# Performance work log

Measured on AMD Instinct MI355X. Metric: run time of the kernel, lower is better.

Reference implementation:

```python
import jax, jax.numpy as jnp
import numpy as np

B, N, H, HID, P = 4, 1024, 16, 64, 2


def setup_inputs() -> dict:
    key = jax.random.key(0)
    ks = jax.random.split(key, 8)
    positions = jax.random.normal(ks[0], (B, N, P), dtype=jnp.float32)
    key_padding_mask = jax.random.bernoulli(ks[1], 0.1, (B, N))
    # MLP params (Linear stores weight as (out,in) in torch; we keep (in,out) and matmul)
    s1 = 1.0 / np.sqrt(P)
    s2 = 1.0 / np.sqrt(HID)
    W1 = jax.random.uniform(ks[2], (P, HID), jnp.float32, -s1, s1)
    b1 = jax.random.uniform(ks[3], (HID,), jnp.float32, -s1, s1)
    W2 = jax.random.uniform(ks[4], (HID, HID), jnp.float32, -s2, s2)
    b2 = jax.random.uniform(ks[5], (HID,), jnp.float32, -s2, s2)
    W3 = jax.random.uniform(ks[6], (HID, H), jnp.float32, -s2, s2)
    b3 = jax.random.uniform(ks[7], (H,), jnp.float32, -s2, s2)
    return {"positions": positions, "key_padding_mask": key_padding_mask,
            "W1": W1, "b1": b1, "W2": W2, "b2": b2, "W3": W3, "b3": b3}


def reference(positions, key_padding_mask, W1, b1, W2, b2, W3, b3):
    # rel_pos[b, i, j] = pos[b, j] - pos[b, i]  -> (B, N, N, 2)
    rel = positions[:, None, :, :] - positions[:, :, None, :]
    h = jax.nn.relu(rel @ W1 + b1)          # (B, N, N, HID)
    h = jax.nn.relu(h @ W2 + b2)            # (B, N, N, HID)
    bias = h @ W3 + b3                      # (B, N, N, H)
    bias = jnp.transpose(bias, (0, 3, 1, 2))  # (B, H, N, N)
    # zero out rows/cols touching padded tokens
    combined = key_padding_mask[:, None, None, :] | key_padding_mask[:, None, :, None]
    bias = jnp.where(combined, 0.0, bias)
    return bias
```

## Files before the change

### kernel.cpp

```cpp
#include <hip/hip_runtime.h>
#include <hip/hip_bf16.h>
#include <hip/hip_fp16.h>

#define B_   4
#define N_   1024
#define H_   16
#define HID_ 64
#define TI   16
#define TJ   128
#define USJ  36

typedef float    f32x4  __attribute__((ext_vector_type(4)));
typedef __fp16   fp16x2 __attribute__((ext_vector_type(2)));
typedef _Float16 f16x8  __attribute__((ext_vector_type(8)));
typedef unsigned int u32;

union F16x8U { u32 u[4]; f16x8 v; };

static __device__ __forceinline__ u32 pk(float a, float b) {
    union { fp16x2 f; u32 u; } r;
    r.f = __builtin_amdgcn_cvt_pkrtz(a, b);
    return r.u;
}
static __device__ __forceinline__ u32 pkadd_relu(u32 a, u32 b) {
    union { u32 u; fp16x2 f; } x, y, r;
    x.u = a; y.u = b;
    fp16x2 z = { (__fp16)0.f, (__fp16)0.f };
    fp16x2 s = x.f + y.f;
    r.f = __builtin_elementwise_max(s, z);
    return r.u;
}
static __device__ __forceinline__ u32 pkcvt_relu(float a, float b) {
    union { fp16x2 f; u32 u; } r;
    fp16x2 z = { (__fp16)0.f, (__fp16)0.f };
    fp16x2 s = __builtin_amdgcn_cvt_pkrtz(a, b);
    r.f = __builtin_elementwise_max(s, z);
    return r.u;
}

__global__ __launch_bounds__(256) void RelativePositionalBias_kernel(
    const float* __restrict__ pos,
    const int*   __restrict__ mask,
    const float* __restrict__ W1,
    const float* __restrict__ b1,
    const float* __restrict__ W2,
    const float* __restrict__ b2,
    const float* __restrict__ W3,
    const float* __restrict__ b3,
    float* __restrict__ out)
{
    __shared__ __align__(16) u32 ujL[TJ][USJ];
    __shared__ __align__(16) u32 uinL[TI][USJ];

    const int b  = blockIdx.z;
    const int i0 = blockIdx.y * TI;
    const int j0 = blockIdx.x * TJ;
    const int tid = threadIdx.x;
    const int w = tid >> 6;
    const int l = tid & 63;
    const int g = l >> 4;
    const int c = l & 15;

    for (int it = tid; it < (TJ + TI) * 8; it += 256) {
        int r  = it >> 3;
        int qq = (it & 7) * 4;
        int k0 = qq * 2;
        int tok = (r < TJ) ? (j0 + r) : (i0 + (r - TJ));
        float2 p  = *(const float2*)&pos[(b * N_ + tok) * 2];
        float4 a0 = *(const float4*)&W1[k0];
        float4 a1 = *(const float4*)&W1[k0 + 4];
        float4 c0 = *(const float4*)&W1[HID_ + k0];
        float4 c1 = *(const float4*)&W1[HID_ + k0 + 4];
        float u0 = p.x*a0.x + p.y*c0.x, u1 = p.x*a0.y + p.y*c0.y;
        float u2 = p.x*a0.z + p.y*c0.z, u3 = p.x*a0.w + p.y*c0.w;
        float u4 = p.x*a1.x + p.y*c1.x, u5 = p.x*a1.y + p.y*c1.y;
        float u6 = p.x*a1.z + p.y*c1.z, u7 = p.x*a1.w + p.y*c1.w;
        uint4 o;
        if (r < TJ) {
            o.x = pk(u0, u1); o.y = pk(u2, u3); o.z = pk(u4, u5); o.w = pk(u6, u7);
            *(uint4*)&ujL[r][qq] = o;
        } else {
            float4 ba = *(const float4*)&b1[k0];
            float4 bb = *(const float4*)&b1[k0 + 4];
            o.x = pk(ba.x - u0, ba.y - u1); o.y = pk(ba.z - u2, ba.w - u3);
            o.z = pk(bb.x - u4, bb.y - u5); o.w = pk(bb.z - u6, bb.w - u7);
            *(uint4*)&uinL[r - TJ][qq] = o;
        }
    }

    F16x8U W2f[2][4];
    #pragma unroll
    for (int s = 0; s < 2; ++s)
        #pragma unroll
        for (int n = 0; n < 4; ++n)
            #pragma unroll
            for (int e = 0; e < 8; ++e)
                W2f[s][n].v[e] = (_Float16)W2[(32*s + 8*g + e) * HID_ + 16*n + c];

    F16x8U W3g[2];
    #pragma unroll
    for (int s = 0; s < 2; ++s)
        #pragma unroll
        for (int e = 0; e < 8; ++e)
            W3g[s].v[e] = (_Float16)W3[(32*s + 16*(e>>2) + 4*g + (e&3)) * H_ + c];

    f32x4 b2v[4];
    #pragma unroll
    for (int n = 0; n < 4; ++n)
        b2v[n] = *(const f32x4*)&b2[16*n + 4*g];

    const float b3v = b3[c];
    const int* maskb = &mask[b * N_ + i0];
    const int4 mj0 = *(const int4*)&mask[b * N_ + j0 + 32*w + 4*g];
    const int4 mj1 = *(const int4*)&mask[b * N_ + j0 + 32*w + 16 + 4*g];
    float* const outBase = out + ((size_t)(b*H_ + c) << 20) + (size_t)(j0 + 32*w + 4*g)
                               + ((size_t)i0 << 10);

    __syncthreads();

    const uint4 pj00 = *(const uint4*)&ujL[32*w + c][4*g];
    const uint4 pj01 = *(const uint4*)&ujL[32*w + c][16 + 4*g];
    const uint4 pj10 = *(const uint4*)&ujL[32*w + 16 + c][4*g];
    const uint4 pj11 = *(const uint4*)&ujL[32*w + 16 + c][16 + 4*g];

    #pragma unroll 2
    for (int t = 0; t < TI; ++t) {
        const int mi = maskb[t];
        float* const outRow = outBase + ((size_t)t << 10);
        f32x4 o0 = { 0.f, 0.f, 0.f, 0.f };
        f32x4 o1 = { 0.f, 0.f, 0.f, 0.f };

        if (!mi) {
            const uint4 uiA = *(const uint4*)&uinL[t][4*g];
            const uint4 uiB = *(const uint4*)&uinL[t][16 + 4*g];

            #pragma unroll
            for (int u = 0; u < 2; ++u) {
                const uint4& pjA = u ? pj10 : pj00;
                const uint4& pjB = u ? pj11 : pj01;

                F16x8U A1[2];
                A1[0].u[0] = pkadd_relu(pjA.x, uiA.x);
                A1[0].u[1] = pkadd_relu(pjA.y, uiA.y);
                A1[0].u[2] = pkadd_relu(pjA.z, uiA.z);
                A1[0].u[3] = pkadd_relu(pjA.w, uiA.w);
                A1[1].u[0] = pkadd_relu(pjB.x, uiB.x);
                A1[1].u[1] = pkadd_relu(pjB.y, uiB.y);
                A1[1].u[2] = pkadd_relu(pjB.z, uiB.z);
                A1[1].u[3] = pkadd_relu(pjB.w, uiB.w);

                f32x4 acc[4];
                #pragma unroll
                for (int n = 0; n < 4; ++n) {
                    acc[n] = __builtin_amdgcn_mfma_f32_16x16x32_f16(W2f[0][n].v, A1[0].v, b2v[n], 0, 0, 0);
                    acc[n] = __builtin_amdgcn_mfma_f32_16x16x32_f16(W2f[1][n].v, A1[1].v, acc[n], 0, 0, 0);
                }

                F16x8U A3[2];
                #pragma unroll
                for (int s = 0; s < 2; ++s) {
                    A3[s].u[0] = pkcvt_relu(acc[2*s][0],     acc[2*s][1]);
                    A3[s].u[1] = pkcvt_relu(acc[2*s][2],     acc[2*s][3]);
                    A3[s].u[2] = pkcvt_relu(acc[2*s + 1][0], acc[2*s + 1][1]);
                    A3[s].u[3] = pkcvt_relu(acc[2*s + 1][2], acc[2*s + 1][3]);
                }

                f32x4 acc3 = { b3v, b3v, b3v, b3v };
                acc3 = __builtin_amdgcn_mfma_f32_16x16x32_f16(A3[0].v, W3g[0].v, acc3, 0, 0, 0);
                acc3 = __builtin_amdgcn_mfma_f32_16x16x32_f16(A3[1].v, W3g[1].v, acc3, 0, 0, 0);

                const int4& mj = u ? mj1 : mj0;
                f32x4& o = u ? o1 : o0;
                o[0] = mj.x ? 0.f : acc3[0];
                o[1] = mj.y ? 0.f : acc3[1];
                o[2] = mj.z ? 0.f : acc3[2];
                o[3] = mj.w ? 0.f : acc3[3];
            }
        }

        *(f32x4*)(outRow)      = o0;
        *(f32x4*)(outRow + 16) = o1;
    }
}

extern "C" void kernel_launch(void* const* d_in, const int* in_sizes, int n_in,
                              void* d_out, int out_size, void* d_ws, size_t ws_size,
                              hipStream_t stream) {
    const float* pos  = (const float*)d_in[0];
    const int*   mask = (const int*)d_in[1];
    const float* W1   = (const float*)d_in[2];
    const float* b1   = (const float*)d_in[3];
    const float* W2   = (const float*)d_in[4];
    const float* b2   = (const float*)d_in[5];
    const float* W3   = (const float*)d_in[6];
    const float* b3   = (const float*)d_in[7];
    float* out = (float*)d_out;

    dim3 grid(N_ / TJ, N_ / TI, B_);
    RelativePositionalBias_kernel<<<grid, dim3(256), 0, stream>>>(
        pos, mask, W1, b1, W2, b2, W3, b3, out);
}
```

Measured before the change: 62.58 us.

## Widen block to full j-row with swizzled LDS layout and bitmask masking

Each block now covers all 1024 j tokens for 16 i rows, using 512 threads. The full j-side layer-1 projections are staged in LDS with an XOR swizzle instead of padding, which cuts the number of blocks and the repeated per-block setup of W2/W3 register fragments. Row masks are packed into a bitmask and column masks become multiplicative factors, and rows where the i token is padded skip straight to zero stores. The trade-offs are larger LDS use (about 130KB), fewer blocks (256) and a request for 2 blocks per CU, which may limit occupancy and make the tail of the grid uneven.

```diff
diff --git a/kernel.cpp b/kernel.cpp
--- a/kernel.cpp
+++ b/kernel.cpp
@@ -7,8 +7,6 @@
 #define H_   16
 #define HID_ 64
 #define TI   16
-#define TJ   128
-#define USJ  36
 
 typedef float    f32x4  __attribute__((ext_vector_type(4)));
 typedef __fp16   fp16x2 __attribute__((ext_vector_type(2)));
@@ -38,7 +36,7 @@
     return r.u;
 }
 
-__global__ __launch_bounds__(256) void RelativePositionalBias_kernel(
+__global__ __launch_bounds__(512, 2) void RelativePositionalBias_kernel(
     const float* __restrict__ pos,
     const int*   __restrict__ mask,
     const float* __restrict__ W1,
@@ -49,23 +47,22 @@
     const float* __restrict__ b3,
     float* __restrict__ out)
 {
-    __shared__ __align__(16) u32 ujL[TJ][USJ];
-    __shared__ __align__(16) u32 uinL[TI][USJ];
-
-    const int b  = blockIdx.z;
-    const int i0 = blockIdx.y * TI;
-    const int j0 = blockIdx.x * TJ;
+    __shared__ __align__(16) u32 ujL[N_][32];
+    __shared__ __align__(16) u32 uinL[TI][32];
+
+    const int b   = blockIdx.y;
+    const int i0  = blockIdx.x * TI;
     const int tid = threadIdx.x;
     const int w = tid >> 6;
     const int l = tid & 63;
     const int g = l >> 4;
     const int c = l & 15;
 
-    for (int it = tid; it < (TJ + TI) * 8; it += 256) {
+    for (int it = tid; it < (N_ + TI) * 8; it += 512) {
         int r  = it >> 3;
-        int qq = (it & 7) * 4;
-        int k0 = qq * 2;
-        int tok = (r < TJ) ? (j0 + r) : (i0 + (r - TJ));
+        int qq = it & 7;
+        int k0 = qq * 8;
+        int tok = (r < N_) ? r : (i0 + (r - N_));
         float2 p  = *(const float2*)&pos[(b * N_ + tok) * 2];
         float4 a0 = *(const float4*)&W1[k0];
         float4 a1 = *(const float4*)&W1[k0 + 4];
@@ -75,16 +72,17 @@
         float u2 = p.x*a0.z + p.y*c0.z, u3 = p.x*a0.w + p.y*c0.w;
         float u4 = p.x*a1.x + p.y*c1.x, u5 = p.x*a1.y + p.y*c1.y;
         float u6 = p.x*a1.z + p.y*c1.z, u7 = p.x*a1.w + p.y*c1.w;
+        const int col = ((qq ^ (r & 7)) << 2);
         uint4 o;
-        if (r < TJ) {
+        if (r < N_) {
             o.x = pk(u0, u1); o.y = pk(u2, u3); o.z = pk(u4, u5); o.w = pk(u6, u7);
-            *(uint4*)&ujL[r][qq] = o;
+            *(uint4*)&ujL[r][col] = o;
         } else {
             float4 ba = *(const float4*)&b1[k0];
             float4 bb = *(const float4*)&b1[k0 + 4];
             o.x = pk(ba.x - u0, ba.y - u1); o.y = pk(ba.z - u2, ba.w - u3);
             o.z = pk(bb.x - u4, bb.y - u5); o.w = pk(bb.z - u6, bb.w - u7);
-            *(uint4*)&uinL[r - TJ][qq] = o;
+            *(uint4*)&uinL[r - N_][col] = o;
         }
     }
 
@@ -108,78 +106,89 @@
     #pragma unroll
     for (int n = 0; n < 4; ++n)
         b2v[n] = *(const f32x4*)&b2[16*n + 4*g];
-
     const float b3v = b3[c];
+
     const int* maskb = &mask[b * N_ + i0];
-    const int4 mj0 = *(const int4*)&mask[b * N_ + j0 + 32*w + 4*g];
-    const int4 mj1 = *(const int4*)&mask[b * N_ + j0 + 32*w + 16 + 4*g];
-    float* const outBase = out + ((size_t)(b*H_ + c) << 20) + (size_t)(j0 + 32*w + 4*g)
-                               + ((size_t)i0 << 10);
+    u32 mrow = 0;
+    #pragma unroll
+    for (int tt = 0; tt < 4; ++tt) {
+        int4 m = *(const int4*)&maskb[tt * 4];
+        mrow |= (m.x ? 1u : 0u) << (4*tt);
+        mrow |= (m.y ? 1u : 0u) << (4*tt + 1);
+        mrow |= (m.z ? 1u : 0u) << (4*tt + 2);
+        mrow |= (m.w ? 1u : 0u) << (4*tt + 3);
+    }
+
+    f32x4 mmul[8];
+    #pragma unroll
+    for (int jj = 0; jj < 8; ++jj) {
+        int4 mj = *(const int4*)&mask[b * N_ + 128*w + 16*jj + 4*g];
+        mmul[jj][0] = mj.x ? 0.f : 1.f;
+        mmul[jj][1] = mj.y ? 0.f : 1.f;
+        mmul[jj][2] = mj.z ? 0.f : 1.f;
+        mmul[jj][3] = mj.w ? 0.f : 1.f;
+    }
+
+    float* const planeBase = out + ((size_t)(b*H_ + c) << 20) + ((size_t)i0 << 10)
+                                 + (size_t)(128*w + 4*g);
 
     __syncthreads();
 
-    const uint4 pj00 = *(const uint4*)&ujL[32*w + c][4*g];
-    const uint4 pj01 = *(const uint4*)&ujL[32*w + c][16 + 4*g];
-    const uint4 pj10 = *(const uint4*)&ujL[32*w + 16 + c][4*g];
-    const uint4 pj11 = *(const uint4*)&ujL[32*w + 16 + c][16 + 4*g];
-
-    #pragma unroll 2
+    const f32x4 zero4 = { 0.f, 0.f, 0.f, 0.f };
+
     for (int t = 0; t < TI; ++t) {
-        const int mi = maskb[t];
-        float* const outRow = outBase + ((size_t)t << 10);
-        f32x4 o0 = { 0.f, 0.f, 0.f, 0.f };
-        f32x4 o1 = { 0.f, 0.f, 0.f, 0.f };
-
-        if (!mi) {
-            const uint4 uiA = *(const uint4*)&uinL[t][4*g];
-            const uint4 uiB = *(const uint4*)&uinL[t][16 + 4*g];
-
-            #pragma unroll
-            for (int u = 0; u < 2; ++u) {
-                const uint4& pjA = u ? pj10 : pj00;
-                const uint4& pjB = u ? pj11 : pj01;
-
-                F16x8U A1[2];
-                A1[0].u[0] = pkadd_relu(pjA.x, uiA.x);
-                A1[0].u[1] = pkadd_relu(pjA.y, uiA.y);
-                A1[0].u[2] = pkadd_relu(pjA.z, uiA.z);
-                A1[0].u[3] = pkadd_relu(pjA.w, uiA.w);
-                A1[1].u[0] = pkadd_relu(pjB.x, uiB.x);
-                A1[1].u[1] = pkadd_relu(pjB.y, uiB.y);
-                A1[1].u[2] = pkadd_relu(pjB.z, uiB.z);
-                A1[1].u[3] = pkadd_relu(pjB.w, uiB.w);
-
-                f32x4 acc[4];
-                #pragma unroll
-                for (int n = 0; n < 4; ++n) {
-                    acc[n] = __builtin_amdgcn_mfma_f32_16x16x32_f16(W2f[0][n].v, A1[0].v, b2v[n], 0, 0, 0);
-                    acc[n] = __builtin_amdgcn_mfma_f32_16x16x32_f16(W2f[1][n].v, A1[1].v, acc[n], 0, 0, 0);
-                }
-
-                F16x8U A3[2];
-                #pragma unroll
-                for (int s = 0; s < 2; ++s) {
-                    A3[s].u[0] = pkcvt_relu(acc[2*s][0],     acc[2*s][1]);
-                    A3[s].u[1] = pkcvt_relu(acc[2*s][2],     acc[2*s][3]);
-                    A3[s].u[2] = pkcvt_relu(acc[2*s + 1][0], acc[2*s + 1][1]);
-                    A3[s].u[3] = pkcvt_relu(acc[2*s + 1][2], acc[2*s + 1][3]);
-                }
-
-                f32x4 acc3 = { b3v, b3v, b3v, b3v };
-                acc3 = __builtin_amdgcn_mfma_f32_16x16x32_f16(A3[0].v, W3g[0].v, acc3, 0, 0, 0);
-                acc3 = __builtin_amdgcn_mfma_f32_16x16x32_f16(A3[1].v, W3g[1].v, acc3, 0, 0, 0);
-
-                const int4& mj = u ? mj1 : mj0;
-                f32x4& o = u ? o1 : o0;
-                o[0] = mj.x ? 0.f : acc3[0];
-                o[1] = mj.y ? 0.f : acc3[1];
-                o[2] = mj.z ? 0.f : acc3[2];
-                o[3] = mj.w ? 0.f : acc3[3];
+        float* const rowp = planeBase + ((size_t)t << 10);
+
+        if ((mrow >> t) & 1) {
+            #pragma unroll
+            for (int jj = 0; jj < 8; ++jj)
+                *(f32x4*)(rowp + 16*jj) = zero4;
+            continue;
+        }
+
+        const int tb = t & 7;
+        const uint4 uiA = *(const uint4*)&uinL[t][(g ^ tb) << 2];
+        const uint4 uiB = *(const uint4*)&uinL[t][((4 + g) ^ tb) << 2];
+
+        #pragma unroll
+        for (int jj = 0; jj < 8; ++jj) {
+            const int jrow = 128*w + 16*jj + c;
+            const int jb = c & 7;
+            const uint4 pjA = *(const uint4*)&ujL[jrow][(g ^ jb) << 2];
+            const uint4 pjB = *(const uint4*)&ujL[jrow][((4 + g) ^ jb) << 2];
+
+            F16x8U A1[2];
+            A1[0].u[0] = pkadd_relu(pjA.x, uiA.x);
+            A1[0].u[1] = pkadd_relu(pjA.y, uiA.y);
+            A1[0].u[2] = pkadd_relu(pjA.z, uiA.z);
+            A1[0].u[3] = pkadd_relu(pjA.w, uiA.w);
+            A1[1].u[0] = pkadd_relu(pjB.x, uiB.x);
+            A1[1].u[1] = pkadd_relu(pjB.y, uiB.y);
+            A1[1].u[2] = pkadd_relu(pjB.z, uiB.z);
+            A1[1].u[3] = pkadd_relu(pjB.w, uiB.w);
+
+            f32x4 acc[4];
+            #pragma unroll
+            for (int n = 0; n < 4; ++n) {
+                acc[n] = __builtin_amdgcn_mfma_f32_16x16x32_f16(W2f[0][n].v, A1[0].v, b2v[n], 0, 0, 0);
+                acc[n] = __builtin_amdgcn_mfma_f32_16x16x32_f16(W2f[1][n].v, A1[1].v, acc[n], 0, 0, 0);
             }
+
+            F16x8U A3[2];
+            #pragma unroll
+            for (int s = 0; s < 2; ++s) {
+                A3[s].u[0] = pkcvt_relu(acc[2*s][0],     acc[2*s][1]);
+                A3[s].u[1] = pkcvt_relu(acc[2*s][2],     acc[2*s][3]);
+                A3[s].u[2] = pkcvt_relu(acc[2*s + 1][0], acc[2*s + 1][1]);
+                A3[s].u[3] = pkcvt_relu(acc[2*s + 1][2], acc[2*s + 1][3]);
+            }
+
+            f32x4 acc3 = { b3v, b3v, b3v, b3v };
+            acc3 = __builtin_amdgcn_mfma_f32_16x16x32_f16(A3[0].v, W3g[0].v, acc3, 0, 0, 0);
+            acc3 = __builtin_amdgcn_mfma_f32_16x16x32_f16(A3[1].v, W3g[1].v, acc3, 0, 0, 0);
+
+            *(f32x4*)(rowp + 16*jj) = acc3 * mmul[jj];
         }
-
-        *(f32x4*)(outRow)      = o0;
-        *(f32x4*)(outRow + 16) = o1;
     }
 }
 
@@ -196,7 +205,7 @@
     const float* b3   = (const float*)d_in[7];
     float* out = (float*)d_out;
 
-    dim3 grid(N_ / TJ, N_ / TI, B_);
-    RelativePositionalBias_kernel<<<grid, dim3(256), 0, stream>>>(
+    dim3 grid(N_ / TI, B_);
+    RelativePositionalBias_kernel<<<grid, dim3(512), 0, stream>>>(
         pos, mask, W1, b1, W2, b2, W3, b3, out);
 }
```

After: 58.88 us. 5.9% less time.
